# Kernel tuning notes

Measured on AMD Instinct MI355X. Metric: run time of the kernel, lower is better.

## Reference

```python
import jax, jax.numpy as jnp
import numpy as np

EMBED_DIM = 1024
ATTN_DIM = 1024


def setup_inputs() -> dict:
    key = jax.random.key(0)
    k1, k2, k3, k4 = jax.random.split(key, 4)
    embedded = jax.random.normal(k1, (4, 2048, EMBED_DIM), dtype=jnp.float32)
    # torch nn.Linear weights are [out_features, in_features]
    s = 1.0 / np.sqrt(EMBED_DIM)
    Wk = jax.random.uniform(k2, (ATTN_DIM, EMBED_DIM), jnp.float32, -s, s)
    Wq = jax.random.uniform(k3, (ATTN_DIM, EMBED_DIM), jnp.float32, -s, s)
    Wv = jax.random.uniform(k4, (ATTN_DIM, EMBED_DIM), jnp.float32, -s, s)
    return {"embedded": embedded, "Wk": Wk, "Wq": Wq, "Wv": Wv}


def reference(embedded, Wk, Wq, Wv):
    # projections: x @ W.T  (torch Linear, no bias)
    k = jnp.einsum("bse,ae->bsa", embedded, Wk)
    q = jnp.einsum("bse,ae->bsa", embedded, Wq)
    v = jnp.einsum("bse,ae->bsa", embedded, Wv)
    scale = 1.0 / jnp.sqrt(jnp.float32(ATTN_DIM))
    attn = jnp.einsum("bqa,bka->bqk", q, k) * scale  # [B, S, S]
    S = attn.shape[1]
    causal = jnp.tril(jnp.ones((S, S), dtype=bool))
    attn = jnp.where(causal[None, :, :], attn, -jnp.inf)
    a = jax.nn.softmax(attn, axis=2)
    out = jnp.einsum("bqk,bka->bqa", a, v)
    return jnp.round(out, 4)
```

## Files before the change

### kernel.cpp

```cpp
#include <hip/hip_runtime.h>
#include <hip/hip_bf16.h>
#include <hip/hip_fp16.h>
#include <stdint.h>

typedef __bf16 bf16_t;
typedef bf16_t bf16x8 __attribute__((ext_vector_type(8)));
typedef bf16_t bf16x4 __attribute__((ext_vector_type(4)));
typedef float f32x4 __attribute__((ext_vector_type(4)));

#define BM 128
#define BN 128
#define BK 32

__device__ __forceinline__ void gload_lds16(const void* g, void* l) {
    __builtin_amdgcn_global_load_lds(
        (const __attribute__((address_space(1))) void*)(uintptr_t)g,
        (__attribute__((address_space(3))) void*)(uintptr_t)l,
        16, 0, 0);
}

template <int EPI>
__device__ __forceinline__ void gemm_body(
    bf16_t* __restrict__ As, bf16_t* __restrict__ Bs,
    const bf16_t* __restrict__ A, long lda,
    const bf16_t* __restrict__ B, long ldb,
    void* __restrict__ Cv, long ldc,
    int k0beg, int k1end, float scale, int m0, int n0,
    float* __restrict__ rs)
{
    const int tid = threadIdx.x;
    const int wid = tid >> 6, lane = tid & 63;
    const int wr = wid >> 1, wc = wid & 1;
    const int hw = lane >> 4, ln = lane & 15;

    const bf16_t *srcA[2], *srcB[2];
#pragma unroll
    for (int i = 0; i < 2; i++) {
        const int c = tid + i * 256;
        const int row = c >> 2;
        const int j = ((c & 3) - (row >> 1)) & 3;
        srcA[i] = A + (size_t)(m0 + row) * lda + j * 8;
        srcB[i] = B + (size_t)(n0 + row) * ldb + j * 8;
    }

    f32x4 acc[4][4] = {};

    for (int k0 = k0beg; k0 < k1end; k0 += BK) {
        gload_lds16(srcA[0] + k0, &As[wid * 512]);
        gload_lds16(srcA[1] + k0, &As[2048 + wid * 512]);
        gload_lds16(srcB[0] + k0, &Bs[wid * 512]);
        gload_lds16(srcB[1] + k0, &Bs[2048 + wid * 512]);
        __syncthreads();

        bf16x8 af[4], bfr[4];
#pragma unroll
        for (int t = 0; t < 4; t++) {
            const int r  = wr * 64 + t * 16 + ln;
            const int rb = wc * 64 + t * 16 + ln;
            af[t]  = *(const bf16x8*)&As[r  * BK + (((hw + (r  >> 1)) & 3) * 8)];
            bfr[t] = *(const bf16x8*)&Bs[rb * BK + (((hw + (rb >> 1)) & 3) * 8)];
        }
#pragma unroll
        for (int ti = 0; ti < 4; ti++)
#pragma unroll
            for (int tj = 0; tj < 4; tj++)
                acc[ti][tj] = __builtin_amdgcn_mfma_f32_16x16x32_bf16(
                    af[ti], bfr[tj], acc[ti][tj], 0, 0, 0);
        __syncthreads();
    }

#pragma unroll
    for (int ti = 0; ti < 4; ti++) {
        const int rbase = m0 + wr * 64 + ti * 16 + hw * 4;
        f32x4 inv4;
        if (EPI == 2) {
            const float4 r4 = *(const float4*)&rs[rbase];
            inv4[0] = 1.0f / r4.x; inv4[1] = 1.0f / r4.y;
            inv4[2] = 1.0f / r4.z; inv4[3] = 1.0f / r4.w;
        }
        float part[4] = {0.f, 0.f, 0.f, 0.f};
#pragma unroll
        for (int tj = 0; tj < 4; tj++) {
            const int col = n0 + wc * 64 + tj * 16 + ln;
            if (EPI == 4) {
                const int bb = rbase >> 11;
                const int s  = rbase & 2047;
                const int d  = col - 2048;
                bf16x4 o;
#pragma unroll
                for (int rg = 0; rg < 4; rg++) o[rg] = (bf16_t)acc[ti][tj][rg];
                *(bf16x4*)&((bf16_t*)Cv)[(size_t)bb * 2097152 + (size_t)d * 2048 + s] = o;
            } else {
#pragma unroll
                for (int rg = 0; rg < 4; rg++) {
                    const size_t idx = (size_t)(rbase + rg) * ldc + col;
                    if (EPI == 0) {
                        ((bf16_t*)Cv)[idx] = (bf16_t)(acc[ti][tj][rg]);
                    } else if (EPI == 2) {
                        ((float*)Cv)[idx] = acc[ti][tj][rg] * inv4[rg];
                    } else {
                        const float e = (col <= rbase + rg)
                                      ? __expf(acc[ti][tj][rg] * scale) : 0.0f;
                        part[rg] += e;
                        ((bf16_t*)Cv)[idx] = (bf16_t)e;
                    }
                }
            }
        }
        if (EPI == 3) {
#pragma unroll
            for (int rg = 0; rg < 4; rg++) {
                float p = part[rg];
                p += __shfl_xor(p, 1, 64);
                p += __shfl_xor(p, 2, 64);
                p += __shfl_xor(p, 4, 64);
                p += __shfl_xor(p, 8, 64);
                if (ln == 0) atomicAdd(&rs[rbase + rg], p);
            }
        }
    }
}

__global__ __launch_bounds__(256) void gemm1_qkv(
    const bf16_t* __restrict__ xb, const bf16_t* __restrict__ Wb,
    bf16_t* __restrict__ QKVb, bf16_t* __restrict__ Vt)
{
    __shared__ __align__(16) bf16_t As[BM * BK];
    __shared__ __align__(16) bf16_t Bs[BN * BK];
    const int lin = blockIdx.x;
    const int xcd = lin & 7;
    const int j   = lin >> 3;
    const int p   = j >> 6;
    const int w   = j & 63;
    const int mblk = xcd * 8 + (w >> 3);
    const int nblk = p * 8 + (w & 7);
    const int m0 = mblk * BM, n0 = nblk * BN;
    if (nblk < 16)
        gemm_body<0>(As, Bs, xb, 1024, Wb, 1024, QKVb, 2048,
                     0, 1024, 1.0f, m0, n0, nullptr);
    else
        gemm_body<4>(As, Bs, xb, 1024, Wb, 1024, Vt, 2048,
                     0, 1024, 1.0f, m0, n0, nullptr);
}

__global__ __launch_bounds__(256) void qk_gemm(
    const bf16_t* __restrict__ QKVb, bf16_t* __restrict__ E,
    float* __restrict__ rowsum)
{
    __shared__ __align__(16) bf16_t As[BM * BK];
    __shared__ __align__(16) bf16_t Bs[BN * BK];
    const int b = blockIdx.x & 3;
    int rem = blockIdx.x >> 2;
    int my = 15, nx = 0;
#pragma unroll
    for (int m = 15; m >= 0; --m) {
        if (rem < m + 1) { my = m; nx = rem; break; }
        rem -= m + 1;
    }
    const bf16_t* base = QKVb + (size_t)b * (2048L * 2048);
    gemm_body<3>(As, Bs,
                 base + 1024, 2048,
                 base, 2048,
                 E + (size_t)b * (2048L * 2048), 2048,
                 0, 1024, 0.03125f, my * BM, nx * BN,
                 rowsum + b * 2048);
}

__global__ __launch_bounds__(256) void gemm3_pv(
    const bf16_t* __restrict__ E, const bf16_t* __restrict__ Vt,
    const float* __restrict__ rowsum, float* __restrict__ out)
{
    __shared__ __align__(16) bf16_t As[BM * BK];
    __shared__ __align__(16) bf16_t Bs[BN * BK];
    const int id = blockIdx.x;
    const int strip = 15 - (id >> 5);
    const int nx = (id >> 2) & 7;
    const int b = id & 3;
    const int m0 = strip * BM;
    gemm_body<2>(As, Bs,
                 E + (size_t)b * (2048L * 2048), 2048,
                 Vt + (size_t)b * (1024L * 2048), 2048,
                 out + (size_t)b * (2048L * 1024), 1024,
                 0, m0 + BM, 1.0f, m0, nx * BN,
                 (float*)rowsum + b * 2048);
}

__global__ __launch_bounds__(256) void cast_all(
    const float* __restrict__ x,
    const float* __restrict__ Wk, const float* __restrict__ Wq,
    const float* __restrict__ Wv,
    bf16_t* __restrict__ xb, bf16_t* __restrict__ Wb,
    float* __restrict__ rowsum)
{
    const int blk = blockIdx.x;
    if (blk >= 11264) {
        const size_t i = ((size_t)(blk - 11264) * 256 + threadIdx.x) * 4;
        *(float4*)(rowsum + i) = make_float4(0.f, 0.f, 0.f, 0.f);
        return;
    }
    const float* src;
    bf16_t* dst;
    if (blk < 8192) {
        const size_t i = ((size_t)blk * 256 + threadIdx.x) * 4;
        src = x + i;
        dst = xb + i;
    } else {
        const size_t j = ((size_t)(blk - 8192) * 256 + threadIdx.x) * 4;
        dst = Wb + j;
        if (j < (size_t)1048576)      src = Wk + j;
        else if (j < (size_t)2097152) src = Wq + (j - 1048576);
        else                          src = Wv + (j - 2097152);
    }
    const float4 v = *(const float4*)src;
    bf16x4 o;
    o.x = (bf16_t)v.x; o.y = (bf16_t)v.y; o.z = (bf16_t)v.z; o.w = (bf16_t)v.w;
    *(bf16x4*)dst = o;
}

extern "C" void kernel_launch(void* const* d_in, const int* in_sizes, int n_in,
                              void* d_out, int out_size, void* d_ws, size_t ws_size,
                              hipStream_t stream)
{
    const float* x  = (const float*)d_in[0];
    const float* Wk = (const float*)d_in[1];
    const float* Wq = (const float*)d_in[2];
    const float* Wv = (const float*)d_in[3];
    char* ws = (char*)d_ws;

    bf16_t* QKVb   = (bf16_t*)(ws);
    bf16_t* Vt     = (bf16_t*)(ws + ((size_t)32 << 20));
    bf16_t* xb     = (bf16_t*)(ws + ((size_t)48 << 20));
    bf16_t* Wb     = (bf16_t*)(ws + ((size_t)64 << 20));
    bf16_t* E      = (bf16_t*)(ws + ((size_t)48 << 20));
    float*  rowsum = (float*)(ws + ((size_t)80 << 20));
    float*  out    = (float*)d_out;

    cast_all<<<11272, 256, 0, stream>>>(x, Wk, Wq, Wv, xb, Wb, rowsum);

    gemm1_qkv<<<1536, 256, 0, stream>>>(xb, Wb, QKVb, Vt);

    qk_gemm<<<544, 256, 0, stream>>>(QKVb, E, rowsum);

    gemm3_pv<<<512, 256, 0, stream>>>(E, Vt, rowsum, out);
}
```

Baseline: 226.2 us.

## Split-K the long causal strips of PV GEMM with atomic accumulation

The PV GEMM now splits each of the lower eight 128-row strips into two K ranges, producing more, smaller blocks with better-balanced work across the causal triangle. Split results are accumulated into the fp32 output with atomicAdd. The cast kernel is extended to pre-zero the affected output rows. This costs extra zeroing writes and atomic traffic and makes the summation order nondeterministic.

```diff
diff --git a/kernel.cpp b/kernel.cpp
--- a/kernel.cpp
+++ b/kernel.cpp
@@ -1,6 +1,5 @@
 #include <hip/hip_runtime.h>
 #include <hip/hip_bf16.h>
-#include <hip/hip_fp16.h>
 #include <stdint.h>
 
 typedef __bf16 bf16_t;
@@ -26,7 +25,7 @@
     const bf16_t* __restrict__ B, long ldb,
     void* __restrict__ Cv, long ldc,
     int k0beg, int k1end, float scale, int m0, int n0,
-    float* __restrict__ rs)
+    float* __restrict__ rs, int use_atomic)
 {
     const int tid = threadIdx.x;
     const int wid = tid >> 6, lane = tid & 63;
@@ -97,7 +96,9 @@
                     if (EPI == 0) {
                         ((bf16_t*)Cv)[idx] = (bf16_t)(acc[ti][tj][rg]);
                     } else if (EPI == 2) {
-                        ((float*)Cv)[idx] = acc[ti][tj][rg] * inv4[rg];
+                        const float v = acc[ti][tj][rg] * inv4[rg];
+                        if (use_atomic) atomicAdd(&((float*)Cv)[idx], v);
+                        else            ((float*)Cv)[idx] = v;
                     } else {
                         const float e = (col <= rbase + rg)
                                       ? __expf(acc[ti][tj][rg] * scale) : 0.0f;
@@ -137,10 +138,10 @@
     const int m0 = mblk * BM, n0 = nblk * BN;
     if (nblk < 16)
         gemm_body<0>(As, Bs, xb, 1024, Wb, 1024, QKVb, 2048,
-                     0, 1024, 1.0f, m0, n0, nullptr);
+                     0, 1024, 1.0f, m0, n0, nullptr, 0);
     else
         gemm_body<4>(As, Bs, xb, 1024, Wb, 1024, Vt, 2048,
-                     0, 1024, 1.0f, m0, n0, nullptr);
+                     0, 1024, 1.0f, m0, n0, nullptr, 0);
 }
 
 __global__ __launch_bounds__(256) void qk_gemm(
@@ -163,7 +164,7 @@
                  base, 2048,
                  E + (size_t)b * (2048L * 2048), 2048,
                  0, 1024, 0.03125f, my * BM, nx * BN,
-                 rowsum + b * 2048);
+                 rowsum + b * 2048, 0);
 }
 
 __global__ __launch_bounds__(256) void gemm3_pv(
@@ -172,17 +173,28 @@
 {
     __shared__ __align__(16) bf16_t As[BM * BK];
     __shared__ __align__(16) bf16_t Bs[BN * BK];
-    const int id = blockIdx.x;
-    const int strip = 15 - (id >> 5);
-    const int nx = (id >> 2) & 7;
-    const int b = id & 3;
-    const int m0 = strip * BM;
+    const int b = blockIdx.x & 3;
+    const int item = blockIdx.x >> 2;
+    int s, nx, k0, k1, at;
+    if (item < 64) {
+        s = item >> 3; nx = item & 7;
+        k0 = 0; k1 = (s + 1) * 128; at = 0;
+    } else {
+        const int q = item - 64;
+        s = 8 + (q >> 4);
+        const int r = q & 15;
+        const int ci = r >> 3;
+        nx = r & 7;
+        k0 = ci ? 1024 : 0;
+        k1 = ci ? (s + 1) * 128 : 1024;
+        at = 1;
+    }
     gemm_body<2>(As, Bs,
                  E + (size_t)b * (2048L * 2048), 2048,
                  Vt + (size_t)b * (1024L * 2048), 2048,
                  out + (size_t)b * (2048L * 1024), 1024,
-                 0, m0 + BM, 1.0f, m0, nx * BN,
-                 (float*)rowsum + b * 2048);
+                 k0, k1, 1.0f, s * BM, nx * BN,
+                 (float*)rowsum + b * 2048, at);
 }
 
 __global__ __launch_bounds__(256) void cast_all(
@@ -190,9 +202,16 @@
     const float* __restrict__ Wk, const float* __restrict__ Wq,
     const float* __restrict__ Wv,
     bf16_t* __restrict__ xb, bf16_t* __restrict__ Wb,
-    float* __restrict__ rowsum)
+    float* __restrict__ rowsum, float* __restrict__ out)
 {
     const int blk = blockIdx.x;
+    if (blk >= 11272) {
+        const int v = blk - 11272;
+        const size_t off = (size_t)(v >> 10) * 2097152 + 1048576
+                         + (size_t)(v & 1023) * 1024 + (size_t)threadIdx.x * 4;
+        *(float4*)(out + off) = make_float4(0.f, 0.f, 0.f, 0.f);
+        return;
+    }
     if (blk >= 11264) {
         const size_t i = ((size_t)(blk - 11264) * 256 + threadIdx.x) * 4;
         *(float4*)(rowsum + i) = make_float4(0.f, 0.f, 0.f, 0.f);
@@ -235,11 +254,11 @@
     float*  rowsum = (float*)(ws + ((size_t)80 << 20));
     float*  out    = (float*)d_out;
 
-    cast_all<<<11272, 256, 0, stream>>>(x, Wk, Wq, Wv, xb, Wb, rowsum);
+    cast_all<<<15368, 256, 0, stream>>>(x, Wk, Wq, Wv, xb, Wb, rowsum, out);
 
     gemm1_qkv<<<1536, 256, 0, stream>>>(xb, Wb, QKVb, Vt);
 
     qk_gemm<<<544, 256, 0, stream>>>(QKVb, E, rowsum);
 
-    gemm3_pv<<<512, 256, 0, stream>>>(E, Vt, rowsum, out);
-}
+    gemm3_pv<<<768, 256, 0, stream>>>(E, Vt, rowsum, out);
+}
```

Result: slower. 232.1 us (+2.6%).
